# Optimization experiments

Hardware: AMD Instinct MI355X
Metric: run time of the kernel (lower is better)

The kernel has to match this reference:

```python
import jax, jax.numpy as jnp
import numpy as np

MARGIN = 0.3

def setup_inputs() -> dict:
    key = jax.random.key(0)
    k1, k2 = jax.random.split(key)
    embeddings = jax.random.normal(k1, (8192, 512), dtype=jnp.float32)
    labels = jax.random.randint(k2, (8192,), 0, 128, dtype=jnp.int64)
    return {"embeddings": embeddings, "labels": labels}

def _pairwise_euclidean(x):
    # ||xi - xj|| via GEMM, matching torch reference (relu clamp + sqrt(.+1e-16))
    dot = x @ x.T                      # [B, B]
    sq = jnp.diagonal(dot)             # [B]
    d2 = sq[None, :] - 2.0 * dot + sq[:, None]
    d2 = jnp.maximum(d2, 0.0)
    return jnp.sqrt(d2 + 1e-16)

def reference(embeddings, labels):
    n = embeddings.shape[0]
    d = _pairwise_euclidean(embeddings)                 # [B, B]
    same = labels[:, None] == labels[None, :]           # [B, B]
    eye = jnp.eye(n, dtype=bool)
    mask_pos = same & ~eye
    mask_neg = ~same
    # fused masked row-wise reductions (hard mining)
    hardest_pos = jnp.max(jnp.where(mask_pos, d, -jnp.inf), axis=1)  # [B]
    hardest_neg = jnp.min(jnp.where(mask_neg, d, jnp.inf), axis=1)   # [B]
    valid = mask_pos.any(axis=1) & mask_neg.any(axis=1)              # [B]
    per_row = jax.nn.relu(hardest_pos - hardest_neg + MARGIN)
    per_row = jnp.where(valid, per_row, 0.0)
    denom = jnp.maximum(jnp.sum(valid.astype(per_row.dtype)), 1.0)
    return jnp.sum(per_row) / denom
```

## Files before the change

kernel.cpp:

```cpp
#include <hip/hip_runtime.h>

#define BATCH 8192
#define DIM   512
#define NTILE 1152

typedef __attribute__((ext_vector_type(4))) float  f32x4;
typedef __attribute__((ext_vector_type(8))) __bf16 bf16x8;

__device__ __forceinline__ unsigned short f2bf(float x) {
  unsigned u = __float_as_uint(x);
  u = (u + 0x7FFFu + ((u >> 16) & 1u)) >> 16;
  return (unsigned short)u;
}

__device__ __forceinline__ void load_lds16(const void* g, void* l) {
  __builtin_amdgcn_global_load_lds(
      (__attribute__((address_space(1))) void*)(g),
      (__attribute__((address_space(3))) void*)(l), 16, 0, 0);
}

template<int N> __device__ __forceinline__ void waitcnt_vm() {
  if constexpr (N == 12)     asm volatile("s_waitcnt vmcnt(12)" ::: "memory");
  else if constexpr (N == 6) asm volatile("s_waitcnt vmcnt(6)"  ::: "memory");
  else if constexpr (N == 3) asm volatile("s_waitcnt vmcnt(3)"  ::: "memory");
  else                       asm volatile("s_waitcnt vmcnt(0)"  ::: "memory");
}

__device__ __forceinline__ void barrier_nofence() {
  asm volatile("" ::: "memory");
  __builtin_amdgcn_s_barrier();
  asm volatile("" ::: "memory");
}

__device__ __forceinline__ unsigned enc(float f) {
  unsigned u = __float_as_uint(f);
  return u ^ (unsigned)(((int)u >> 31) | 0x80000000);
}
__device__ __forceinline__ float dec(unsigned k) {
  unsigned u = (k & 0x80000000u) ? (k ^ 0x80000000u) : ~k;
  return __uint_as_float(u);
}

__global__ __launch_bounds__(256) void prep_kernel(
    const float* __restrict__ X, unsigned short* __restrict__ Xb,
    float* __restrict__ sq, unsigned* __restrict__ ctrl,
    uint4* __restrict__ pos4, uint4* __restrict__ neg4) {
  int gid = blockIdx.x * 256 + threadIdx.x;
  if (gid == 0) {
    ((float*)ctrl)[0] = 0.f;
    ((float*)ctrl)[1] = 0.f;
    ctrl[2] = 0u;
    ctrl[3] = 0u;
  }
  if (gid < 196608) {
    pos4[gid] = (uint4){0u, 0u, 0u, 0u};
    neg4[gid] = (uint4){~0u, ~0u, ~0u, ~0u};
  }
  int wave = threadIdx.x >> 6, lane = threadIdx.x & 63;
  int row = blockIdx.x * 4 + wave;
  const float4* xr = (const float4*)(X + (size_t)row * DIM);
  float4 a = xr[lane * 2];
  float4 b = xr[lane * 2 + 1];
  float s = a.x*a.x + a.y*a.y + a.z*a.z + a.w*a.w
          + b.x*b.x + b.y*b.y + b.z*b.z + b.w*b.w;
  uint4 p;
  p.x = (unsigned)f2bf(a.x) | ((unsigned)f2bf(a.y) << 16);
  p.y = (unsigned)f2bf(a.z) | ((unsigned)f2bf(a.w) << 16);
  p.z = (unsigned)f2bf(b.x) | ((unsigned)f2bf(b.y) << 16);
  p.w = (unsigned)f2bf(b.z) | ((unsigned)f2bf(b.w) << 16);
  ((uint4*)(Xb + (size_t)row * DIM))[lane] = p;
  #pragma unroll
  for (int off = 32; off > 0; off >>= 1) s += __shfl_down(s, off);
  if (lane == 0) sq[row] = s;
}

template<int NI>
__device__ __forceinline__ void stage(
    const unsigned short* __restrict__ Xb, int i0, int jw, int k,
    unsigned short* buf, int wave, int lane) {
  int r4 = lane >> 2;
  int sc = (lane & 3) ^ (r4 & 3);
  int koff = k + sc * 8;
  #pragma unroll
  for (int tt = 0; tt < 2; tt++) {
    int c = wave * 2 + tt;
    load_lds16(Xb + (size_t)(i0 + c * 16 + r4) * DIM + koff, buf + c * 512);
  }
  constexpr int NB = NI / 2;
  #pragma unroll
  for (int tt = 0; tt < NB; tt++) {
    int c = wave * NB + tt;
    load_lds16(Xb + (size_t)(jw + c * 16 + r4) * DIM + koff, buf + 4096 + c * 512);
  }
}

template<int NI>
__device__ __forceinline__ void gemm_tile(
    const unsigned short* __restrict__ Xb, int i0, int jw,
    unsigned short* r0, unsigned short* r1, unsigned short* r2,
    int wave, int wm, int wn, int quad, int lc, int lane,
    f32x4 (&acc)[4][8]) {
  constexpr int S = 2 + NI / 2;
  unsigned short *bc = r0, *bn = r1, *bt = r2;
  stage<NI>(Xb, i0, jw, 0,  bc, wave, lane);
  stage<NI>(Xb, i0, jw, 32, bn, wave, lane);
  int aoff = (quad ^ (lc & 3)) * 8;
  for (int t = 0; t < 16; t++) {
    if (t < 14) {
      stage<NI>(Xb, i0, jw, (t + 2) * 32, bt, wave, lane);
      waitcnt_vm<2 * S>();
    } else if (t == 14) {
      waitcnt_vm<S>();
    } else {
      waitcnt_vm<0>();
    }
    barrier_nofence();
    bf16x8 af[4], bfr[NI];
    #pragma unroll
    for (int mi = 0; mi < 4; mi++)
      af[mi] = *(const bf16x8*)&bc[(wm * 64 + mi * 16 + lc) * 32 + aoff];
    #pragma unroll
    for (int ni = 0; ni < NI; ni++)
      bfr[ni] = *(const bf16x8*)&bc[4096 + (wn * (NI * 16) + ni * 16 + lc) * 32 + aoff];
    #pragma unroll
    for (int mi = 0; mi < 4; mi++)
      #pragma unroll
      for (int ni = 0; ni < NI; ni++)
        acc[mi][ni] = __builtin_amdgcn_mfma_f32_16x16x32_bf16(
            af[mi], bfr[ni], acc[mi][ni], 0, 0, 0);
    barrier_nofence();
    unsigned short* tp = bc; bc = bn; bn = bt; bt = tp;
  }
}

template<bool STRAD, int NI, int WNS>
__device__ __forceinline__ void epilogue(
    const f32x4 (&acc)[4][8], const float* __restrict__ sq,
    const int* __restrict__ labels,
    int i0, int jwin, int wm, int wn, int quad, int lc,
    unsigned (*ibuf)[128][2], unsigned (*jbuf)[256][2]) {
  float sqj_r[NI]; int labj_r[NI];
  #pragma unroll
  for (int ni = 0; ni < NI; ni++) {
    int j = jwin + wn * WNS + ni * 16 + lc;
    sqj_r[ni] = sq[j]; labj_r[ni] = labels[j];
  }
  float rpos[16], rneg[16];
  float jp[NI], jn[NI];
  #pragma unroll
  for (int x = 0; x < NI; x++) { jp[x] = -3e38f; jn[x] = 3e38f; }
  #pragma unroll
  for (int mi = 0; mi < 4; mi++) {
    #pragma unroll
    for (int r = 0; r < 4; r++) {
      int ig = i0 + wm * 64 + mi * 16 + quad * 4 + r;
      int li = labels[ig];
      float si = sq[ig];
      float rp = -3e38f, rn = 3e38f;
      #pragma unroll
      for (int ni = 0; ni < NI; ni++) {
        float a = acc[mi][ni][r];
        float v = fmaf(-2.f, a, sqj_r[ni]);
        bool same = (li == labj_r[ni]);
        bool posok = same;
        if (STRAD) posok = same && ((jwin + wn * WNS + ni * 16 + lc) != ig);
        rp = fmaxf(rp, posok ? v : -3e38f);
        rn = fminf(rn, same ? 3e38f : v);
        if (!STRAD) {
          float v2 = fmaf(-2.f, a, si);
          jp[ni] = fmaxf(jp[ni], same ? v2 : -3e38f);
          jn[ni] = fminf(jn[ni], same ? 3e38f : v2);
        }
      }
      rpos[mi * 4 + r] = rp; rneg[mi * 4 + r] = rn;
    }
  }
  #pragma unroll
  for (int m = 1; m <= 8; m <<= 1)
    #pragma unroll
    for (int x = 0; x < 16; x++) {
      rpos[x] = fmaxf(rpos[x], __shfl_xor(rpos[x], m));
      rneg[x] = fminf(rneg[x], __shfl_xor(rneg[x], m));
    }
  if (lc == 0) {
    #pragma unroll
    for (int mi = 0; mi < 4; mi++)
      #pragma unroll
      for (int r = 0; r < 4; r++) {
        int row = wm * 64 + mi * 16 + quad * 4 + r;
        ibuf[wn][row][0] = enc(rpos[mi * 4 + r]);
        ibuf[wn][row][1] = enc(rneg[mi * 4 + r]);
      }
  }
  if (!STRAD) {
    #pragma unroll
    for (int m = 16; m <= 32; m <<= 1)
      #pragma unroll
      for (int x = 0; x < NI; x++) {
        jp[x] = fmaxf(jp[x], __shfl_xor(jp[x], m));
        jn[x] = fminf(jn[x], __shfl_xor(jn[x], m));
      }
    if (quad == 0) {
      #pragma unroll
      for (int ni = 0; ni < NI; ni++) {
        int col = wn * WNS + ni * 16 + lc;
        jbuf[wm][col][0] = enc(jp[ni]);
        jbuf[wm][col][1] = enc(jn[ni]);
      }
    }
  }
}

__global__ __launch_bounds__(256, 2) void triplet_mfma(
    const unsigned short* __restrict__ Xb, const float* __restrict__ sq,
    const int* __restrict__ labels, unsigned* __restrict__ ctrl,
    unsigned* __restrict__ pos_i, unsigned* __restrict__ neg_i,
    unsigned* __restrict__ pos_j, unsigned* __restrict__ neg_j) {
  __shared__ __align__(16) unsigned short ring[3][12288];
  __shared__ int tshare;

  unsigned (*ibuf)[128][2] = reinterpret_cast<unsigned (*)[128][2]>(&ring[0][0]);
  unsigned (*jbuf)[256][2] = reinterpret_cast<unsigned (*)[256][2]>(&ring[0][1024]);

  int tid = threadIdx.x;
  int wave = tid >> 6, lane = tid & 63;
  int wm = wave >> 1, wn = wave & 1;
  int quad = lane >> 4, lc = lane & 15;

  for (;;) {
    if (tid == 0) tshare = (int)atomicAdd(&ctrl[3], 1u);
    __syncthreads();
    int t = tshare;
    if (t >= NTILE) break;

    int It = 0, Js = 0, q = -1; bool strad = false;
    if (t < 64) { It = t; Js = t >> 1; strad = true; }
    else {
      int u;
      if (t < 1024) u = t - 64;
      else { q = (t - 1024) & 3; u = 960 + ((t - 1024) >> 2); }
      for (int s = 0; s < 64; s++) {
        int c = 31 - (s >> 1);
        if (u < c) { It = s; Js = (s >> 1) + 1 + u; break; }
        u -= c;
      }
    }
    int i0 = It * 128;
    int jw = Js * 256 + (q >= 0 ? q * 64 : 0);

    f32x4 acc[4][8];
    #pragma unroll
    for (int mi = 0; mi < 4; mi++)
      #pragma unroll
      for (int ni = 0; ni < 8; ni++)
        acc[mi][ni] = (f32x4){0.f, 0.f, 0.f, 0.f};

    if (q >= 0) {
      gemm_tile<2>(Xb, i0, jw, ring[0], ring[1], ring[2],
                   wave, wm, wn, quad, lc, lane, acc);
      epilogue<false, 2, 32>(acc, sq, labels, i0, jw, wm, wn, quad, lc, ibuf, jbuf);
    } else {
      gemm_tile<8>(Xb, i0, jw, ring[0], ring[1], ring[2],
                   wave, wm, wn, quad, lc, lane, acc);
      if (strad)
        epilogue<true, 8, 128>(acc, sq, labels, i0, jw, wm, wn, quad, lc, ibuf, jbuf);
      else
        epilogue<false, 8, 128>(acc, sq, labels, i0, jw, wm, wn, quad, lc, ibuf, jbuf);
    }
    __syncthreads();

    if (q >= 0) {
      if (tid < 128) {
        unsigned p = max(ibuf[0][tid][0], ibuf[1][tid][0]);
        unsigned n = min(ibuf[0][tid][1], ibuf[1][tid][1]);
        atomicMax(&pos_i[(size_t)Js * BATCH + i0 + tid], p);
        atomicMin(&neg_i[(size_t)Js * BATCH + i0 + tid], n);
      }
      if (tid < 64) {
        unsigned p = max(jbuf[0][tid][0], jbuf[1][tid][0]);
        unsigned n = min(jbuf[0][tid][1], jbuf[1][tid][1]);
        pos_j[(size_t)It * BATCH + jw + tid] = p;
        neg_j[(size_t)It * BATCH + jw + tid] = n;
      }
    } else {
      if (tid < 128) {
        unsigned p = max(ibuf[0][tid][0], ibuf[1][tid][0]);
        unsigned n = min(ibuf[0][tid][1], ibuf[1][tid][1]);
        pos_i[(size_t)Js * BATCH + i0 + tid] = p;
        neg_i[(size_t)Js * BATCH + i0 + tid] = n;
      }
      if (!strad) {
        unsigned p = max(jbuf[0][tid][0], jbuf[1][tid][0]);
        unsigned n = min(jbuf[0][tid][1], jbuf[1][tid][1]);
        pos_j[(size_t)It * BATCH + jw + tid] = p;
        neg_j[(size_t)It * BATCH + jw + tid] = n;
      }
    }
    __syncthreads();
  }
}

__global__ __launch_bounds__(256) void final_kernel(
    const unsigned* __restrict__ pos_i, const unsigned* __restrict__ neg_i,
    const unsigned* __restrict__ pos_j, const unsigned* __restrict__ neg_j,
    const float* __restrict__ sq, unsigned* __restrict__ ctrl,
    float* __restrict__ out) {
  int i = blockIdx.x * 256 + threadIdx.x;
  unsigned pe = 0u, ne = 0xFFFFFFFFu;
  #pragma unroll 4
  for (int s = 0; s < 32; s++) {
    pe = max(pe, pos_i[(size_t)s * BATCH + i]);
    ne = min(ne, neg_i[(size_t)s * BATCH + i]);
  }
  #pragma unroll 4
  for (int s = 0; s < 64; s++) {
    pe = max(pe, pos_j[(size_t)s * BATCH + i]);
    ne = min(ne, neg_j[(size_t)s * BATCH + i]);
  }
  float p = dec(pe), n = dec(ne);
  float term = 0.f, cnt = 0.f;
  if (p > -1e37f && n < 1e37f) {
    float si = sq[i];
    float dp = sqrtf(fmaxf(si + p, 0.f) + 1e-16f);
    float dn = sqrtf(fmaxf(si + n, 0.f) + 1e-16f);
    term = fmaxf(dp - dn + 0.3f, 0.f);
    cnt = 1.f;
  }
  #pragma unroll
  for (int off = 32; off > 0; off >>= 1) {
    term += __shfl_down(term, off);
    cnt  += __shfl_down(cnt, off);
  }
  __shared__ float ss[4], sc[4];
  int wave = threadIdx.x >> 6, lane = threadIdx.x & 63;
  if (lane == 0) { ss[wave] = term; sc[wave] = cnt; }
  __syncthreads();
  if (threadIdx.x == 0) {
    atomicAdd((float*)&ctrl[0], ss[0] + ss[1] + ss[2] + ss[3]);
    atomicAdd((float*)&ctrl[1], sc[0] + sc[1] + sc[2] + sc[3]);
    __threadfence();
    unsigned t = atomicAdd(&ctrl[2], 1u);
    if (t == 31u) {
      float S = atomicAdd((float*)&ctrl[0], 0.f);
      float C = atomicAdd((float*)&ctrl[1], 0.f);
      out[0] = S / fmaxf(C, 1.f);
    }
  }
}

extern "C" void kernel_launch(void* const* d_in, const int* in_sizes, int n_in,
                              void* d_out, int out_size, void* d_ws, size_t ws_size,
                              hipStream_t stream) {
  const float* X      = (const float*)d_in[0];
  const int*   labels = (const int*)d_in[1];
  float* out = (float*)d_out;
  char* ws = (char*)d_ws;

  const size_t SLOT = (size_t)BATCH * 4;
  unsigned short* Xb = (unsigned short*)ws;
  float* sq      = (float*)(ws + (8u << 20));
  unsigned* ctrl = (unsigned*)(ws + (8u << 20) + (32u << 10));
  char*  posb = ws + (8u << 20) + (64u << 10);
  char*  negb = posb + 96 * SLOT;
  unsigned* pos_i = (unsigned*)posb;
  unsigned* pos_j = (unsigned*)(posb + 32 * SLOT);
  unsigned* neg_i = (unsigned*)negb;
  unsigned* neg_j = (unsigned*)(negb + 32 * SLOT);

  prep_kernel<<<BATCH / 4, 256, 0, stream>>>(X, Xb, sq, ctrl,
                                             (uint4*)posb, (uint4*)negb);
  triplet_mfma<<<512, 256, 0, stream>>>(Xb, sq, labels, ctrl,
                                        pos_i, neg_i, pos_j, neg_j);
  final_kernel<<<BATCH / 256, 256, 0, stream>>>(pos_i, neg_i, pos_j, neg_j, sq, ctrl, out);
}
```

Before: 142.3 us.

## Switch GEMM LDS ring from triple to double buffering with new swizzle layout

Replaces the three-stage LDS ring, which waited on partial vmcnt counts, with a two-buffer scheme that issues the next k-slice load, computes on the current one, then waits for all loads and barriers. It also changes the LDS row/column mapping and XOR swizzle so each 16-row chunk stores pairs of rows per 64-element line, aiming to cut bank conflicts on the bf16x8 fragment reads. Shared memory drops by one buffer, which may allow more resident blocks, but only one slice is prefetched ahead and every iteration drains the global load queue completely.

```diff
diff --git a/kernel.cpp b/kernel.cpp
--- a/kernel.cpp
+++ b/kernel.cpp
@@ -19,17 +19,13 @@
       (__attribute__((address_space(3))) void*)(l), 16, 0, 0);
 }
 
-template<int N> __device__ __forceinline__ void waitcnt_vm() {
-  if constexpr (N == 12)     asm volatile("s_waitcnt vmcnt(12)" ::: "memory");
-  else if constexpr (N == 6) asm volatile("s_waitcnt vmcnt(6)"  ::: "memory");
-  else if constexpr (N == 3) asm volatile("s_waitcnt vmcnt(3)"  ::: "memory");
-  else                       asm volatile("s_waitcnt vmcnt(0)"  ::: "memory");
-}
-
 __device__ __forceinline__ void barrier_nofence() {
   asm volatile("" ::: "memory");
   __builtin_amdgcn_s_barrier();
   asm volatile("" ::: "memory");
+}
+__device__ __forceinline__ void wait_vm0() {
+  asm volatile("s_waitcnt vmcnt(0)" ::: "memory");
 }
 
 __device__ __forceinline__ unsigned enc(float f) {
@@ -78,58 +74,57 @@
 __device__ __forceinline__ void stage(
     const unsigned short* __restrict__ Xb, int i0, int jw, int k,
     unsigned short* buf, int wave, int lane) {
-  int r4 = lane >> 2;
-  int sc = (lane & 3) ^ (r4 & 3);
-  int koff = k + sc * 8;
+  int p = lane >> 3;
+  int h = (lane >> 2) & 1;
+  int r = p * 2 + h;
+  int c = (lane & 3) ^ (p & 3);
+  int koff = k + c * 8;
   #pragma unroll
   for (int tt = 0; tt < 2; tt++) {
-    int c = wave * 2 + tt;
-    load_lds16(Xb + (size_t)(i0 + c * 16 + r4) * DIM + koff, buf + c * 512);
+    int cb = wave * 2 + tt;
+    load_lds16(Xb + (size_t)(i0 + cb * 16 + r) * DIM + koff, buf + cb * 512);
   }
   constexpr int NB = NI / 2;
   #pragma unroll
   for (int tt = 0; tt < NB; tt++) {
-    int c = wave * NB + tt;
-    load_lds16(Xb + (size_t)(jw + c * 16 + r4) * DIM + koff, buf + 4096 + c * 512);
+    int cb = wave * NB + tt;
+    load_lds16(Xb + (size_t)(jw + cb * 16 + r) * DIM + koff, buf + 4096 + cb * 512);
   }
 }
 
 template<int NI>
 __device__ __forceinline__ void gemm_tile(
     const unsigned short* __restrict__ Xb, int i0, int jw,
-    unsigned short* r0, unsigned short* r1, unsigned short* r2,
+    unsigned short* b0, unsigned short* b1,
     int wave, int wm, int wn, int quad, int lc, int lane,
     f32x4 (&acc)[4][8]) {
-  constexpr int S = 2 + NI / 2;
-  unsigned short *bc = r0, *bn = r1, *bt = r2;
-  stage<NI>(Xb, i0, jw, 0,  bc, wave, lane);
-  stage<NI>(Xb, i0, jw, 32, bn, wave, lane);
-  int aoff = (quad ^ (lc & 3)) * 8;
+  stage<NI>(Xb, i0, jw, 0, b0, wave, lane);
+  wait_vm0();
+  barrier_nofence();
+  int rbase = (lc >> 1) * 64 + (lc & 1) * 32;
+  int csw   = (quad ^ ((lc >> 1) & 3)) * 8;
+  unsigned short* bc = b0;
+  unsigned short* bn = b1;
   for (int t = 0; t < 16; t++) {
-    if (t < 14) {
-      stage<NI>(Xb, i0, jw, (t + 2) * 32, bt, wave, lane);
-      waitcnt_vm<2 * S>();
-    } else if (t == 14) {
-      waitcnt_vm<S>();
-    } else {
-      waitcnt_vm<0>();
-    }
-    barrier_nofence();
+    if (t < 15) stage<NI>(Xb, i0, jw, (t + 1) * 32, bn, wave, lane);
     bf16x8 af[4], bfr[NI];
     #pragma unroll
     for (int mi = 0; mi < 4; mi++)
-      af[mi] = *(const bf16x8*)&bc[(wm * 64 + mi * 16 + lc) * 32 + aoff];
+      af[mi] = *(const bf16x8*)&bc[(wm * 4 + mi) * 512 + rbase + csw];
     #pragma unroll
     for (int ni = 0; ni < NI; ni++)
-      bfr[ni] = *(const bf16x8*)&bc[4096 + (wn * (NI * 16) + ni * 16 + lc) * 32 + aoff];
+      bfr[ni] = *(const bf16x8*)&bc[4096 + (wn * NI + ni) * 512 + rbase + csw];
     #pragma unroll
     for (int mi = 0; mi < 4; mi++)
       #pragma unroll
       for (int ni = 0; ni < NI; ni++)
         acc[mi][ni] = __builtin_amdgcn_mfma_f32_16x16x32_bf16(
             af[mi], bfr[ni], acc[mi][ni], 0, 0, 0);
-    barrier_nofence();
-    unsigned short* tp = bc; bc = bn; bn = bt; bt = tp;
+    if (t < 15) {
+      wait_vm0();
+      barrier_nofence();
+    }
+    unsigned short* tp = bc; bc = bn; bn = tp;
   }
 }
 
@@ -216,7 +211,7 @@
     const int* __restrict__ labels, unsigned* __restrict__ ctrl,
     unsigned* __restrict__ pos_i, unsigned* __restrict__ neg_i,
     unsigned* __restrict__ pos_j, unsigned* __restrict__ neg_j) {
-  __shared__ __align__(16) unsigned short ring[3][12288];
+  __shared__ __align__(16) unsigned short ring[2][12288];
   __shared__ int tshare;
 
   unsigned (*ibuf)[128][2] = reinterpret_cast<unsigned (*)[128][2]>(&ring[0][0]);
@@ -256,12 +251,10 @@
         acc[mi][ni] = (f32x4){0.f, 0.f, 0.f, 0.f};
 
     if (q >= 0) {
-      gemm_tile<2>(Xb, i0, jw, ring[0], ring[1], ring[2],
-                   wave, wm, wn, quad, lc, lane, acc);
+      gemm_tile<2>(Xb, i0, jw, ring[0], ring[1], wave, wm, wn, quad, lc, lane, acc);
       epilogue<false, 2, 32>(acc, sq, labels, i0, jw, wm, wn, quad, lc, ibuf, jbuf);
     } else {
-      gemm_tile<8>(Xb, i0, jw, ring[0], ring[1], ring[2],
-                   wave, wm, wn, quad, lc, lane, acc);
+      gemm_tile<8>(Xb, i0, jw, ring[0], ring[1], wave, wm, wn, quad, lc, lane, acc);
       if (strad)
         epilogue<true, 8, 128>(acc, sq, labels, i0, jw, wm, wn, quad, lc, ibuf, jbuf);
       else
```

New measurement: 139.4 us. -2.0%, faster.
